# Performance work log

Measured on AMD Instinct MI355X. Metric: run time of the kernel, lower is better.

## Reference

```python
import jax, jax.numpy as jnp
import numpy as np

N, DIM_IN, DIM_V, VH, VW, H = 2048, 256, 256, 7, 7, 64
NK = VH * VW
DIM_Q = DIM_V * H  # 16384
EPS = 1e-5


def layer_norm(x, g, b):
    m = jnp.mean(x, axis=-1, keepdims=True)
    var = jnp.mean((x - m) ** 2, axis=-1, keepdims=True)
    return (x - m) / jnp.sqrt(var + EPS) * g + b


def setup_inputs() -> dict:
    key = jax.random.key(0)
    ks = jax.random.split(key, 6)
    x = jax.random.normal(ks[0], (N, DIM_IN), dtype=jnp.float32)
    v = jax.random.normal(ks[1], (N, DIM_V, NK), dtype=jnp.float32)
    Wq_w = jax.random.normal(ks[2], (2 * DIM_Q, DIM_IN), dtype=jnp.float32) * 0.02
    Wq_b = jnp.zeros((2 * DIM_Q,), dtype=jnp.float32)
    Wv_w = jax.random.normal(ks[3], (DIM_IN, DIM_V * NK), dtype=jnp.float32) * 0.02
    Wv_b = jnp.zeros((DIM_IN,), dtype=jnp.float32)
    return {
        "x": x, "v": v,
        "Wq_w": Wq_w, "Wq_b": Wq_b,
        "ln0_g": jnp.ones((H,), jnp.float32), "ln0_b": jnp.zeros((H,), jnp.float32),
        "ln1_g": jnp.ones((DIM_V,), jnp.float32), "ln1_b": jnp.zeros((DIM_V,), jnp.float32),
        "Wv_w": Wv_w, "Wv_b": Wv_b,
        "lnv_g": jnp.ones((DIM_IN,), jnp.float32), "lnv_b": jnp.zeros((DIM_IN,), jnp.float32),
        "lnf_g": jnp.ones((DIM_IN,), jnp.float32), "lnf_b": jnp.zeros((DIM_IN,), jnp.float32),
    }


def reference(x, v, Wq_w, Wq_b, ln0_g, ln0_b, ln1_g, ln1_b, Wv_w, Wv_b, lnv_g, lnv_b, lnf_g, lnf_b):
    n = x.shape[0]
    vt = jnp.transpose(v, (0, 2, 1))                      # [N, Nk, V]
    q = x @ Wq_w.T + Wq_b                                 # [N, 2*dim_q]
    # dynamic_conv_num == 2: two bmm stages with per-sample weights from q
    p1 = q[:, :DIM_Q].reshape(n, DIM_V, H)                # [N, V, H]
    t = jnp.einsum('nkv,nvh->nkh', vt, p1)                # [N, Nk, H]
    t = jax.nn.relu(layer_norm(t, ln0_g, ln0_b))
    p2 = q[:, DIM_Q:].reshape(n, H, DIM_V)                # [N, H, V]
    t = jnp.einsum('nkh,nhv->nkv', t, p2)                 # [N, Nk, V]
    t = jax.nn.relu(layer_norm(t, ln1_g, ln1_b))
    flat = t.reshape(n, NK * DIM_V)                       # [N, Nk*V]
    w = jax.nn.relu(layer_norm(flat @ Wv_w.T + Wv_b, lnv_g, lnv_b))  # [N, dim_in]
    return layer_norm(x + w, lnf_g, lnf_b)
```

## Files before the change

### kernel.cpp

```cpp
#include <hip/hip_runtime.h>

#define LN_EPS 1e-5f


typedef __attribute__((ext_vector_type(8))) short short8;
typedef __attribute__((ext_vector_type(16))) float f32x16;

__global__ __launch_bounds__(256) void k0_split(
    const float* __restrict__ in, ushort* __restrict__ hi,
    ushort* __restrict__ lo, int n4)
{
    const int i = blockIdx.x * 256 + threadIdx.x;
    if (i >= n4) return;
    const float4 f = ((const float4*)in)[i];
    const uint ux = __float_as_uint(f.x), uy = __float_as_uint(f.y);
    const uint uz = __float_as_uint(f.z), uw = __float_as_uint(f.w);
    ushort4 h, l;
    h.x = (ushort)(ux >> 16); h.y = (ushort)(uy >> 16);
    h.z = (ushort)(uz >> 16); h.w = (ushort)(uw >> 16);
    l.x = (ushort)(__float_as_uint(f.x - __uint_as_float(ux & 0xffff0000u)) >> 16);
    l.y = (ushort)(__float_as_uint(f.y - __uint_as_float(uy & 0xffff0000u)) >> 16);
    l.z = (ushort)(__float_as_uint(f.z - __uint_as_float(uz & 0xffff0000u)) >> 16);
    l.w = (ushort)(__float_as_uint(f.w - __uint_as_float(uw & 0xffff0000u)) >> 16);
    ((ushort4*)hi)[i] = h;
    ((ushort4*)lo)[i] = l;
}

template<bool HAS_BIAS>
__global__ __launch_bounds__(256, 2) void gemm_sb3(
    const ushort* __restrict__ Ah, const ushort* __restrict__ Al,
    const float* __restrict__ B, const float* __restrict__ bias,
    float* __restrict__ C, int lda, int ldb, int ldc,
    size_t cSplitStride, int kPerSplit)
{
    __shared__ __align__(16) ushort sAh[8192];
    __shared__ __align__(16) ushort sAl[8192];
    __shared__ __align__(16) ushort sBh[8192];
    __shared__ __align__(16) ushort sBl[8192];

    const int tid = threadIdx.x;
    const int m0 = blockIdx.x << 7;
    const int j0 = blockIdx.y << 7;
    const int ks0 = blockIdx.z * kPerSplit;
    float* Cb = C + (size_t)blockIdx.z * cSplitStride;

    const int lane = tid & 63;
    const int wid = tid >> 6;
    const int wr = wid >> 1;
    const int wc = wid & 1;
    const int swz = (lane & 7) << 3;
    const int rA = (wr << 6) + (lane & 31);
    const int rB = (wc << 6) + (lane & 31);
    const int khalf = (lane >> 5) << 3;

    f32x16 acc[2][2];
#pragma unroll
    for (int r = 0; r < 2; ++r)
#pragma unroll
        for (int c = 0; c < 2; ++c)
#pragma unroll
            for (int e = 0; e < 16; ++e) acc[r][c][e] = 0.f;

    for (int kg0 = 0; kg0 < kPerSplit; kg0 += 64) {
        const int kg = ks0 + kg0;

        uint4 av[8];
#pragma unroll
        for (int p = 0; p < 2; ++p) {
            const ushort* src = p ? Al : Ah;
#pragma unroll
            for (int i = 0; i < 4; ++i) {
                const int id = tid + (i << 8);
                const int row = id >> 3;
                const int c8 = (id & 7) << 3;
                av[p * 4 + i] = *(const uint4*)(src + (size_t)(m0 + row) * lda + kg + c8);
            }
        }
        float4 bv[8];
#pragma unroll
        for (int i = 0; i < 8; ++i) {
            const int id = tid + (i << 8);
            const int row = id >> 4;
            const int c4 = (id & 15) << 2;
            bv[i] = *(const float4*)(B + (size_t)(j0 + row) * ldb + kg + c4);
        }

        if (kg0 > 0) __syncthreads();

#pragma unroll
        for (int p = 0; p < 2; ++p) {
            ushort* dst = p ? sAl : sAh;
#pragma unroll
            for (int i = 0; i < 4; ++i) {
                const int id = tid + (i << 8);
                const int row = id >> 3;
                const int c8 = (id & 7) << 3;
                *(uint4*)&dst[((row << 6) + c8) ^ ((row & 7) << 3)] = av[p * 4 + i];
            }
        }
#pragma unroll
        for (int i = 0; i < 8; ++i) {
            const int id = tid + (i << 8);
            const int row = id >> 4;
            const int c4 = (id & 15) << 2;
            const uint ux = __float_as_uint(bv[i].x), uy = __float_as_uint(bv[i].y);
            const uint uz = __float_as_uint(bv[i].z), uw = __float_as_uint(bv[i].w);
            const float lx = bv[i].x - __uint_as_float(ux & 0xffff0000u);
            const float ly = bv[i].y - __uint_as_float(uy & 0xffff0000u);
            const float lz = bv[i].z - __uint_as_float(uz & 0xffff0000u);
            const float lw = bv[i].w - __uint_as_float(uw & 0xffff0000u);
            const uint h01 = (ux >> 16) | (uy & 0xffff0000u);
            const uint h23 = (uz >> 16) | (uw & 0xffff0000u);
            const uint l01 = (__float_as_uint(lx) >> 16) | (__float_as_uint(ly) & 0xffff0000u);
            const uint l23 = (__float_as_uint(lz) >> 16) | (__float_as_uint(lw) & 0xffff0000u);
            const int sidx = ((row << 6) + c4) ^ ((row & 7) << 3);
            *(uint2*)&sBh[sidx] = make_uint2(h01, h23);
            *(uint2*)&sBl[sidx] = make_uint2(l01, l23);
        }
        __syncthreads();

#pragma unroll
        for (int ks = 0; ks < 4; ++ks) {
            const int kf = (ks << 4) + khalf;
            const int ia0 = ((rA << 6) + kf) ^ swz;
            const int ia1 = (((rA + 32) << 6) + kf) ^ swz;
            const int ib0 = ((rB << 6) + kf) ^ swz;
            const int ib1 = (((rB + 32) << 6) + kf) ^ swz;
            const short8 a0h = *(const short8*)&sAh[ia0];
            const short8 a0l = *(const short8*)&sAl[ia0];
            const short8 a1h = *(const short8*)&sAh[ia1];
            const short8 a1l = *(const short8*)&sAl[ia1];
            const short8 b0h = *(const short8*)&sBh[ib0];
            const short8 b0l = *(const short8*)&sBl[ib0];
            const short8 b1h = *(const short8*)&sBh[ib1];
            const short8 b1l = *(const short8*)&sBl[ib1];

            acc[0][0] = __builtin_amdgcn_mfma_f32_32x32x16_bf16(a0h, b0h, acc[0][0], 0, 0, 0);
            acc[0][1] = __builtin_amdgcn_mfma_f32_32x32x16_bf16(a0h, b1h, acc[0][1], 0, 0, 0);
            acc[1][0] = __builtin_amdgcn_mfma_f32_32x32x16_bf16(a1h, b0h, acc[1][0], 0, 0, 0);
            acc[1][1] = __builtin_amdgcn_mfma_f32_32x32x16_bf16(a1h, b1h, acc[1][1], 0, 0, 0);
            acc[0][0] = __builtin_amdgcn_mfma_f32_32x32x16_bf16(a0h, b0l, acc[0][0], 0, 0, 0);
            acc[0][1] = __builtin_amdgcn_mfma_f32_32x32x16_bf16(a0h, b1l, acc[0][1], 0, 0, 0);
            acc[1][0] = __builtin_amdgcn_mfma_f32_32x32x16_bf16(a1h, b0l, acc[1][0], 0, 0, 0);
            acc[1][1] = __builtin_amdgcn_mfma_f32_32x32x16_bf16(a1h, b1l, acc[1][1], 0, 0, 0);
            acc[0][0] = __builtin_amdgcn_mfma_f32_32x32x16_bf16(a0l, b0h, acc[0][0], 0, 0, 0);
            acc[0][1] = __builtin_amdgcn_mfma_f32_32x32x16_bf16(a0l, b1h, acc[0][1], 0, 0, 0);
            acc[1][0] = __builtin_amdgcn_mfma_f32_32x32x16_bf16(a1l, b0h, acc[1][0], 0, 0, 0);
            acc[1][1] = __builtin_amdgcn_mfma_f32_32x32x16_bf16(a1l, b1h, acc[1][1], 0, 0, 0);
        }
    }

#pragma unroll
    for (int rb = 0; rb < 2; ++rb)
#pragma unroll
        for (int cb = 0; cb < 2; ++cb) {
            const int col = j0 + (wc << 6) + (cb << 5) + (lane & 31);
            const float bvv = HAS_BIAS ? bias[col] : 0.0f;
            const int rbase = m0 + (wr << 6) + (rb << 5) + ((lane >> 5) << 2);
            float* cp = Cb + (size_t)rbase * ldc + col;
#pragma unroll
            for (int reg = 0; reg < 16; ++reg) {
                const int rr = (reg & 3) + ((reg >> 2) << 3);
                cp[(size_t)rr * ldc] = acc[rb][cb][reg] + bvv;
            }
        }
}

__global__ __launch_bounds__(512, 4) void k2_dynconv(
    const float* __restrict__ v, const float* __restrict__ q,
    const float* __restrict__ ln0g, const float* __restrict__ ln0b,
    const float* __restrict__ ln1g, const float* __restrict__ ln1b,
    ushort* __restrict__ fhi, ushort* __restrict__ flo)
{
    __shared__ __align__(16) float sm[10756];
    float* const thL = sm;
    float* const vL  = sm + 3332;
    float* const pL  = sm + 6660;

    const int n = blockIdx.x;
    const int tid = threadIdx.x;
    const float* vrow = v + (size_t)n * 12544;
    const float* qrow = q + (size_t)n * 32768;

    const int ktA = tid >> 4;
    const int h0A = (tid & 15) << 2;
    float ta[4][4];
#pragma unroll
    for (int r = 0; r < 4; ++r)
#pragma unroll
        for (int c = 0; c < 4; ++c) ta[r][c] = 0.f;

    for (int ch = 0; ch < 4; ++ch) {
        if (ch) __syncthreads();
        for (int i4 = tid; i4 < 784; i4 += 512) {
            const float4 f = *(const float4*)(vrow + ch * 3136 + (i4 << 2));
            const int base = i4 << 2;
#pragma unroll
            for (int e = 0; e < 4; ++e) {
                const int idx = base + e;
                const int dv = (int)(((uint)idx * 85599u) >> 22);
                const int k = idx - dv * 49;
                vL[dv * 52 + k] = ((const float*)&f)[e];
            }
        }
        for (int i = tid; i < 1024; i += 512)
            *(float4*)&pL[i << 2] = *(const float4*)(qrow + (ch << 12) + (i << 2));
        __syncthreads();

        if (tid < 208) {
#pragma unroll 2
            for (int dv = 0; dv < 64; ++dv) {
                const float4 a4 = *(const float4*)&vL[dv * 52 + (ktA << 2)];
                const float4 b4 = *(const float4*)&pL[(dv << 6) + h0A];
                const float* ap = (const float*)&a4;
                const float* bp = (const float*)&b4;
#pragma unroll
                for (int r = 0; r < 4; ++r)
#pragma unroll
                    for (int c = 0; c < 4; ++c)
                        ta[r][c] = fmaf(ap[r], bp[c], ta[r][c]);
            }
        }
    }

    if (tid < 208) {
        float s1[4], s2[4];
#pragma unroll
        for (int r = 0; r < 4; ++r) {
            s1[r] = ta[r][0] + ta[r][1] + ta[r][2] + ta[r][3];
            s2[r] = ta[r][0]*ta[r][0] + ta[r][1]*ta[r][1]
                  + ta[r][2]*ta[r][2] + ta[r][3]*ta[r][3];
        }
#pragma unroll
        for (int m = 1; m < 16; m <<= 1)
#pragma unroll
            for (int r = 0; r < 4; ++r) {
                s1[r] += __shfl_xor(s1[r], m);
                s2[r] += __shfl_xor(s2[r], m);
            }
        const float4 g4 = *(const float4*)&ln0g[h0A];
        const float4 b4 = *(const float4*)&ln0b[h0A];
        const float* gp = (const float*)&g4;
        const float* bp = (const float*)&b4;
#pragma unroll
        for (int r = 0; r < 4; ++r) {
            const int k = (ktA << 2) + r;
            if (k < 49) {
                const float mean = s1[r] * (1.f / 64.f);
                const float var = s2[r] * (1.f / 64.f) - mean * mean;
                const float rstd = rsqrtf(var + LN_EPS);
                float4 o;
                o.x = fmaxf((ta[r][0] - mean) * rstd * gp[0] + bp[0], 0.f);
                o.y = fmaxf((ta[r][1] - mean) * rstd * gp[1] + bp[1], 0.f);
                o.z = fmaxf((ta[r][2] - mean) * rstd * gp[2] + bp[2], 0.f);
                o.w = fmaxf((ta[r][3] - mean) * rstd * gp[3] + bp[3], 0.f);
                *(float4*)&thL[k * 68 + h0A] = o;
            }
        }
    }
    __syncthreads();

    const int ktB = tid >> 5;
    const int j0B = (tid & 31) << 3;
    const int g0 = (tid & 31) << 1;
    const int sw0 = (g0 ^ (g0 >> 3)) << 2;
    const int sw1 = ((g0 + 1) ^ ((g0 + 1) >> 3)) << 2;
    int roffB[4];
#pragma unroll
    for (int r = 0; r < 4; ++r) {
        const int k = (ktB << 2) + r;
        roffB[r] = (k < 49 ? k : 48) * 68;
    }
    float acc[4][8];
#pragma unroll
    for (int r = 0; r < 4; ++r)
#pragma unroll
        for (int c = 0; c < 8; ++c) acc[r][c] = 0.f;

    for (int ch = 0; ch < 4; ++ch) {
        if (ch) __syncthreads();
        for (int i = tid; i < 1024; i += 512) {
            const int h = i >> 6;
            const int g = i & 63;
            const int s = g ^ (g >> 3);
            *(float4*)&pL[(h << 8) + (s << 2)] =
                *(const float4*)(qrow + 16384 + (ch << 12) + (i << 2));
        }
        __syncthreads();

        if (tid < 416) {
#pragma unroll
            for (int hb = 0; hb < 4; ++hb) {
                float4 a4[4];
#pragma unroll
                for (int r = 0; r < 4; ++r)
                    a4[r] = *(const float4*)&thL[roffB[r] + (ch << 4) + (hb << 2)];
#pragma unroll
                for (int hh = 0; hh < 4; ++hh) {
                    const int hl = (hb << 2) + hh;
                    const float4 b0 = *(const float4*)&pL[(hl << 8) + sw0];
                    const float4 b1 = *(const float4*)&pL[(hl << 8) + sw1];
                    const float* bp0 = (const float*)&b0;
                    const float* bp1 = (const float*)&b1;
#pragma unroll
                    for (int r = 0; r < 4; ++r) {
                        const float a = ((const float*)&a4[r])[hh];
#pragma unroll
                        for (int c = 0; c < 4; ++c) {
                            acc[r][c]     = fmaf(a, bp0[c], acc[r][c]);
                            acc[r][c + 4] = fmaf(a, bp1[c], acc[r][c + 4]);
                        }
                    }
                }
            }
        }
    }

    if (tid < 416) {
        float s1[4], s2[4];
#pragma unroll
        for (int r = 0; r < 4; ++r) {
            float a1 = 0.f, a2 = 0.f;
#pragma unroll
            for (int c = 0; c < 8; ++c) { a1 += acc[r][c]; a2 += acc[r][c] * acc[r][c]; }
            s1[r] = a1; s2[r] = a2;
        }
#pragma unroll
        for (int m = 1; m < 32; m <<= 1)
#pragma unroll
            for (int r = 0; r < 4; ++r) {
                s1[r] += __shfl_xor(s1[r], m);
                s2[r] += __shfl_xor(s2[r], m);
            }
        const float4 g0v = *(const float4*)&ln1g[j0B];
        const float4 g1v = *(const float4*)&ln1g[j0B + 4];
        const float4 b0v = *(const float4*)&ln1b[j0B];
        const float4 b1v = *(const float4*)&ln1b[j0B + 4];
        const float* gp = (const float*)&g0v;
        const float* gq = (const float*)&g1v;
        const float* bp = (const float*)&b0v;
        const float* bq = (const float*)&b1v;
#pragma unroll
        for (int r = 0; r < 4; ++r) {
            const int k = (ktB << 2) + r;
            if (k < 49) {
                const float mean = s1[r] * (1.f / 256.f);
                const float var = s2[r] * (1.f / 256.f) - mean * mean;
                const float rstd = rsqrtf(var + LN_EPS);
                float o[8];
#pragma unroll
                for (int c = 0; c < 4; ++c) {
                    o[c]     = fmaxf((acc[r][c]     - mean) * rstd * gp[c] + bp[c], 0.f);
                    o[c + 4] = fmaxf((acc[r][c + 4] - mean) * rstd * gq[c] + bq[c], 0.f);
                }
                ushort4 h4a, h4b, l4a, l4b;
#pragma unroll
                for (int c = 0; c < 4; ++c) {
                    const uint u = __float_as_uint(o[c]);
                    ((ushort*)&h4a)[c] = (ushort)(u >> 16);
                    ((ushort*)&l4a)[c] = (ushort)(__float_as_uint(o[c] - __uint_as_float(u & 0xffff0000u)) >> 16);
                    const uint u2 = __float_as_uint(o[c + 4]);
                    ((ushort*)&h4b)[c] = (ushort)(u2 >> 16);
                    ((ushort*)&l4b)[c] = (ushort)(__float_as_uint(o[c + 4] - __uint_as_float(u2 & 0xffff0000u)) >> 16);
                }
                const size_t fo = (size_t)n * 12544 + k * 256 + j0B;
                *(ushort4*)&fhi[fo] = h4a;
                *(ushort4*)&fhi[fo + 4] = h4b;
                *(ushort4*)&flo[fo] = l4a;
                *(ushort4*)&flo[fo + 4] = l4b;
            }
        }
    }
}

__global__ __launch_bounds__(256) void k4_final(
    const float* __restrict__ wpart, const float* __restrict__ x,
    const float* __restrict__ Wvb,
    const float* __restrict__ lnvg, const float* __restrict__ lnvb,
    const float* __restrict__ lnfg, const float* __restrict__ lnfb,
    float* __restrict__ out)
{
    const int n = (blockIdx.x << 2) + (threadIdx.x >> 6);
    const int lane = threadIdx.x & 63;
    const int j = lane << 2;

    float a0 = 0.f, a1 = 0.f, a2 = 0.f, a3 = 0.f;
#pragma unroll
    for (int s = 0; s < 14; ++s) {
        const float4 p = *(const float4*)&wpart[((size_t)s * 2048 + n) * 256 + j];
        a0 += p.x; a1 += p.y; a2 += p.z; a3 += p.w;
    }
    const float4 bb = *(const float4*)&Wvb[j];
    a0 += bb.x; a1 += bb.y; a2 += bb.z; a3 += bb.w;

    float s1 = a0 + a1 + a2 + a3;
    float s2 = a0*a0 + a1*a1 + a2*a2 + a3*a3;
#pragma unroll
    for (int off = 32; off > 0; off >>= 1) {
        s1 += __shfl_xor(s1, off);
        s2 += __shfl_xor(s2, off);
    }
    float m = s1 * (1.f / 256.f);
    float var = s2 * (1.f / 256.f) - m * m;
    float rr = rsqrtf(var + LN_EPS);
    const float4 g = *(const float4*)&lnvg[j];
    const float4 b = *(const float4*)&lnvb[j];
    const float w0 = fmaxf((a0 - m) * rr * g.x + b.x, 0.f);
    const float w1 = fmaxf((a1 - m) * rr * g.y + b.y, 0.f);
    const float w2 = fmaxf((a2 - m) * rr * g.z + b.z, 0.f);
    const float w3 = fmaxf((a3 - m) * rr * g.w + b.w, 0.f);

    const float4 xv = *(const float4*)&x[(size_t)n * 256 + j];
    const float t0 = xv.x + w0, t1 = xv.y + w1, t2 = xv.z + w2, t3 = xv.w + w3;
    s1 = t0 + t1 + t2 + t3;
    s2 = t0*t0 + t1*t1 + t2*t2 + t3*t3;
#pragma unroll
    for (int off = 32; off > 0; off >>= 1) {
        s1 += __shfl_xor(s1, off);
        s2 += __shfl_xor(s2, off);
    }
    m = s1 * (1.f / 256.f);
    var = s2 * (1.f / 256.f) - m * m;
    rr = rsqrtf(var + LN_EPS);
    const float4 gf = *(const float4*)&lnfg[j];
    const float4 bf = *(const float4*)&lnfb[j];
    float4 o;
    o.x = (t0 - m) * rr * gf.x + bf.x;
    o.y = (t1 - m) * rr * gf.y + bf.y;
    o.z = (t2 - m) * rr * gf.z + bf.z;
    o.w = (t3 - m) * rr * gf.w + bf.w;
    *(float4*)&out[(size_t)n * 256 + j] = o;
}

extern "C" void kernel_launch(void* const* d_in, const int* in_sizes, int n_in,
                              void* d_out, int out_size, void* d_ws, size_t ws_size,
                              hipStream_t stream)
{
    const float* x    = (const float*)d_in[0];
    const float* v    = (const float*)d_in[1];
    const float* Wq_w = (const float*)d_in[2];
    const float* Wq_b = (const float*)d_in[3];
    const float* ln0g = (const float*)d_in[4];
    const float* ln0b = (const float*)d_in[5];
    const float* ln1g = (const float*)d_in[6];
    const float* ln1b = (const float*)d_in[7];
    const float* Wv_w = (const float*)d_in[8];
    const float* Wv_b = (const float*)d_in[9];
    const float* lnvg = (const float*)d_in[10];
    const float* lnvb = (const float*)d_in[11];
    const float* lnfg = (const float*)d_in[12];
    const float* lnfb = (const float*)d_in[13];
    float* out = (float*)d_out;

    if (ws_size < 371195904ull) return;
    char* ws = (char*)d_ws;
    float* q        = (float*)ws;
    ushort* flat_hi = (ushort*)(ws + 268435456u);
    ushort* flat_lo = (ushort*)(ws + 319815680u);
    ushort* xs_hi   = (ushort*)(ws + 268435456u);
    ushort* xs_lo   = xs_hi + 524288;
    float* wpart    = q;

    k0_split<<<512, 256, 0, stream>>>(x, xs_hi, xs_lo, 131072);

    gemm_sb3<true><<<dim3(16, 256, 1), 256, 0, stream>>>(
        xs_hi, xs_lo, Wq_w, Wq_b, q, 256, 256, 32768, 0, 256);

    k2_dynconv<<<2048, 512, 0, stream>>>(v, q, ln0g, ln0b, ln1g, ln1b,
                                         flat_hi, flat_lo);

    gemm_sb3<false><<<dim3(16, 2, 14), 256, 0, stream>>>(
        flat_hi, flat_lo, Wv_w, nullptr, wpart, 12544, 12544, 256,
        (size_t)2048 * 256, 896);

    k4_final<<<512, 256, 0, stream>>>(wpart, x, Wv_b, lnvg, lnvb, lnfg, lnfb, out);
}
```

Before: 803.4 us.

## Remap GEMM blocks across XCDs and coalesce epilogue stores through LDS

```diff
diff --git a/kernel.cpp b/kernel.cpp
--- a/kernel.cpp
+++ b/kernel.cpp
@@ -31,18 +31,25 @@
     const ushort* __restrict__ Ah, const ushort* __restrict__ Al,
     const float* __restrict__ B, const float* __restrict__ bias,
     float* __restrict__ C, int lda, int ldb, int ldc,
-    size_t cSplitStride, int kPerSplit)
+    size_t cSplitStride, int kPerSplit, int nJT)
 {
-    __shared__ __align__(16) ushort sAh[8192];
-    __shared__ __align__(16) ushort sAl[8192];
-    __shared__ __align__(16) ushort sBh[8192];
-    __shared__ __align__(16) ushort sBl[8192];
+    __shared__ __align__(16) ushort smem[32768];
+    ushort* const sAh = smem;
+    ushort* const sAl = smem + 8192;
+    ushort* const sBh = smem + 16384;
+    ushort* const sBl = smem + 24576;
 
     const int tid = threadIdx.x;
-    const int m0 = blockIdx.x << 7;
-    const int j0 = blockIdx.y << 7;
-    const int ks0 = blockIdx.z * kPerSplit;
-    float* Cb = C + (size_t)blockIdx.z * cSplitStride;
+    const int nwg8 = (int)gridDim.x >> 3;
+    const int id = (int)blockIdx.x;
+    const int nid = (id & 7) * nwg8 + (id >> 3);
+    const int mT = nid & 15;
+    const int jT = (nid >> 4) % nJT;
+    const int sT = (nid >> 4) / nJT;
+    const int m0 = mT << 7;
+    const int j0 = jT << 7;
+    const int ks0 = sT * kPerSplit;
+    float* Cb = C + (size_t)sT * cSplitStride;
 
     const int lane = tid & 63;
     const int wid = tid >> 6;
@@ -70,18 +77,18 @@
             const ushort* src = p ? Al : Ah;
 #pragma unroll
             for (int i = 0; i < 4; ++i) {
-                const int id = tid + (i << 8);
-                const int row = id >> 3;
-                const int c8 = (id & 7) << 3;
+                const int idx = tid + (i << 8);
+                const int row = idx >> 3;
+                const int c8 = (idx & 7) << 3;
                 av[p * 4 + i] = *(const uint4*)(src + (size_t)(m0 + row) * lda + kg + c8);
             }
         }
         float4 bv[8];
 #pragma unroll
         for (int i = 0; i < 8; ++i) {
-            const int id = tid + (i << 8);
-            const int row = id >> 4;
-            const int c4 = (id & 15) << 2;
+            const int idx = tid + (i << 8);
+            const int row = idx >> 4;
+            const int c4 = (idx & 15) << 2;
             bv[i] = *(const float4*)(B + (size_t)(j0 + row) * ldb + kg + c4);
         }
 
@@ -92,17 +99,17 @@
             ushort* dst = p ? sAl : sAh;
 #pragma unroll
             for (int i = 0; i < 4; ++i) {
-                const int id = tid + (i << 8);
-                const int row = id >> 3;
-                const int c8 = (id & 7) << 3;
+                const int idx = tid + (i << 8);
+                const int row = idx >> 3;
+                const int c8 = (idx & 7) << 3;
                 *(uint4*)&dst[((row << 6) + c8) ^ ((row & 7) << 3)] = av[p * 4 + i];
             }
         }
 #pragma unroll
         for (int i = 0; i < 8; ++i) {
-            const int id = tid + (i << 8);
-            const int row = id >> 4;
-            const int c4 = (id & 15) << 2;
+            const int idx = tid + (i << 8);
+            const int row = idx >> 4;
+            const int c4 = (idx & 15) << 2;
             const uint ux = __float_as_uint(bv[i].x), uy = __float_as_uint(bv[i].y);
             const uint uz = __float_as_uint(bv[i].z), uw = __float_as_uint(bv[i].w);
             const float lx = bv[i].x - __uint_as_float(ux & 0xffff0000u);
@@ -150,20 +157,32 @@
         }
     }
 
+    __syncthreads();
+    float* cbuf = (float*)smem + (wid << 12);
 #pragma unroll
     for (int rb = 0; rb < 2; ++rb)
 #pragma unroll
         for (int cb = 0; cb < 2; ++cb) {
-            const int col = j0 + (wc << 6) + (cb << 5) + (lane & 31);
-            const float bvv = HAS_BIAS ? bias[col] : 0.0f;
-            const int rbase = m0 + (wr << 6) + (rb << 5) + ((lane >> 5) << 2);
-            float* cp = Cb + (size_t)rbase * ldc + col;
+            const int c = (cb << 5) + (lane & 31);
+            const int r0 = (rb << 5) + ((lane >> 5) << 2);
 #pragma unroll
             for (int reg = 0; reg < 16; ++reg) {
                 const int rr = (reg & 3) + ((reg >> 2) << 3);
-                cp[(size_t)rr * ldc] = acc[rb][cb][reg] + bvv;
-            }
-        }
+                cbuf[((r0 + rr) << 6) + c] = acc[rb][cb][reg];
+            }
+        }
+    const int colq = (lane & 15) << 2;
+    const int rsub = lane >> 4;
+    const int gc = j0 + (wc << 6) + colq;
+    float4 bb = make_float4(0.f, 0.f, 0.f, 0.f);
+    if (HAS_BIAS) bb = *(const float4*)&bias[gc];
+#pragma unroll
+    for (int it = 0; it < 16; ++it) {
+        const int rl = (it << 2) + rsub;
+        float4 val = *(const float4*)&cbuf[(rl << 6) + colq];
+        val.x += bb.x; val.y += bb.y; val.z += bb.z; val.w += bb.w;
+        *(float4*)(Cb + (size_t)(m0 + (wr << 6) + rl) * ldc + gc) = val;
+    }
 }
 
 __global__ __launch_bounds__(512, 4) void k2_dynconv(
@@ -463,15 +482,15 @@
 
     k0_split<<<512, 256, 0, stream>>>(x, xs_hi, xs_lo, 131072);
 
-    gemm_sb3<true><<<dim3(16, 256, 1), 256, 0, stream>>>(
-        xs_hi, xs_lo, Wq_w, Wq_b, q, 256, 256, 32768, 0, 256);
+    gemm_sb3<true><<<4096, 256, 0, stream>>>(
+        xs_hi, xs_lo, Wq_w, Wq_b, q, 256, 256, 32768, 0, 256, 256);
 
     k2_dynconv<<<2048, 512, 0, stream>>>(v, q, ln0g, ln0b, ln1g, ln1b,
                                          flat_hi, flat_lo);
 
-    gemm_sb3<false><<<dim3(16, 2, 14), 256, 0, stream>>>(
+    gemm_sb3<false><<<448, 256, 0, stream>>>(
         flat_hi, flat_lo, Wv_w, nullptr, wpart, 12544, 12544, 256,
-        (size_t)2048 * 256, 896);
+        (size_t)2048 * 256, 896, 2);
 
     k4_final<<<512, 256, 0, stream>>>(wpart, x, Wv_b, lnvg, lnvb, lnfg, lnfb, out);
 }
```

Result: faster. 735.6 us (-8.4%).
